# Performance work log

Measured on AMD Instinct MI355X. Metric: run time of the kernel, lower is better.

## Reference

```python
import jax, jax.numpy as jnp
import numpy as np

KERNEL_NUM = 21
SIGMA = 0.1
EXACT_SIGMA = 0.001
EPS = 1e-8  # torch F.cosine_similarity eps


def _kernel_params():
    n = KERNEL_NUM - 1
    mus = [1.0 / n + 2.0 * i / n - 1.0 for i in range(n)] + [1.0]
    sigmas = [SIGMA] * n + [EXACT_SIGMA]
    return jnp.asarray(mus, jnp.float32), jnp.asarray(sigmas, jnp.float32)


def setup_inputs() -> dict:
    key = jax.random.key(0)
    ks = jax.random.split(key, 12)
    B, QL, DL, V, D = 512, 32, 256, 100000, 256
    return {
        "query_1": jax.random.randint(ks[0], (B, QL), 0, V),
        "document_1": jax.random.randint(ks[1], (B, DL), 0, V),
        "query_2": jax.random.randint(ks[2], (B, QL), 0, V),
        "document_2": jax.random.randint(ks[3], (B, DL), 0, V),
        "emb_weight": jax.random.normal(ks[4], (V, D), jnp.float32),
        "W0": jax.random.normal(ks[5], (10, 21), jnp.float32) * 0.2,
        "b0": jax.random.normal(ks[6], (10,), jnp.float32) * 0.1,
        "W1": jax.random.normal(ks[7], (5, 10), jnp.float32) * 0.3,
        "b1": jax.random.normal(ks[8], (5,), jnp.float32) * 0.1,
        "W2": jax.random.normal(ks[9], (1, 5), jnp.float32) * 0.4,
        "b2": jax.random.normal(ks[10], (1,), jnp.float32) * 0.1,
    }


def _predict(query, doc, emb_weight, W0, b0, W1, b1, W2, b2):
    q = emb_weight[query]  # [B, QL, D]
    d = emb_weight[doc]    # [B, DL, D]
    qn = q / jnp.maximum(jnp.linalg.norm(q, axis=-1, keepdims=True), EPS)
    dn = d / jnp.maximum(jnp.linalg.norm(d, axis=-1, keepdims=True), EPS)
    mm = jnp.einsum('bqe,bde->bqd', qn, dn)  # cosine matching matrix [B,QL,DL]
    mus, sigmas = _kernel_params()
    # Gaussian soft binning: [B,QL,DL,K]
    K = jnp.exp(-0.5 * (mm[..., None] - mus) ** 2 / sigmas ** 2)
    km = jnp.log1p(K.sum(axis=2)).sum(axis=1)  # [B, K]
    h = jax.nn.relu(km @ W0.T + b0)
    h = jax.nn.relu(h @ W1.T + b1)
    return h @ W2.T + b2  # [B, 1]


def reference(query_1, document_1, query_2, document_2,
              emb_weight, W0, b0, W1, b1, W2, b2):
    l1 = _predict(query_1, document_1, emb_weight, W0, b0, W1, b1, W2, b2)
    l2 = _predict(query_2, document_2, emb_weight, W0, b0, W1, b1, W2, b2)
    return jax.nn.sigmoid(l1 - l2)
```

## Files before the change

kernel.cpp:

```cpp
#include <hip/hip_runtime.h>
#include <hip/hip_fp8.h>
#include <math.h>

typedef __bf16 bf16x8 __attribute__((ext_vector_type(8)));
typedef __bf16 bf16x4 __attribute__((ext_vector_type(4)));
typedef float  f32x4  __attribute__((ext_vector_type(4)));
typedef float  f32x16 __attribute__((ext_vector_type(16)));

#define QL    32
#define DL    256
#define DIM   256
#define NK    21
#define KSOFT 20
#define STR   264
#define STR8  264
#define L2E   1.4426950408889634f

#if __has_builtin(__builtin_amdgcn_exp2f)
#define EXP2F(x) __builtin_amdgcn_exp2f(x)
#else
#define EXP2F(x) exp2f(x)
#endif

static __device__ inline unsigned cvt2_e4m3(float a, float b)
{
#if __has_builtin(__builtin_amdgcn_cvt_pk_fp8_f32)
    return (unsigned)__builtin_amdgcn_cvt_pk_fp8_f32(a, b, 0, false) & 0xFFFFu;
#else
    __hip_fp8_e4m3 fa(a), fb(b);
    return (unsigned)fa.__x | ((unsigned)fb.__x << 8);
#endif
}

#define EVAL_BINS(mm, ACC0)                                                  \
    {                                                                        \
        float U  = EXP2F(L2E * fmaf(10.0f, (mm), 9.0f));                     \
        float t0 = (mm) + 0.95f;                                             \
        float E  = EXP2F((-50.0f * L2E) * t0 * t0);                          \
        ACC0[0] += E;                                                        \
        E *= U;                           ACC0[1]  += E;          \
        E *= U * 0.36787944117144233f;    ACC0[2]  += E;          \
        E *= U * 0.1353352832366127f;     ACC0[3]  += E;          \
        E *= U * 0.049787068367863944f;   ACC0[4]  += E;          \
        E *= U * 0.018315638888734179f;   ACC0[5]  += E;          \
        E *= U * 0.006737946999085467f;   ACC0[6]  += E;          \
        float t7 = (mm) + 0.25f;                                             \
        E = EXP2F((-50.0f * L2E) * t7 * t7);                                 \
        ACC0[7] += E;                                                        \
        E *= U * 0.0009118819655545162f;  ACC0[8]  += E;          \
        E *= U * 0.00033546262790251185f; ACC0[9]  += E;          \
        E *= U * 0.0001234098040866796f;  ACC0[10] += E;          \
        E *= U * 4.5399929762484854e-05f; ACC0[11] += E;          \
        E *= U * 1.670170079024566e-05f;  ACC0[12] += E;          \
        E *= U * 6.14421235332821e-06f;   ACC0[13] += E;          \
        float t14 = (mm) - 0.45f;                                            \
        E = EXP2F((-50.0f * L2E) * t14 * t14);                               \
        ACC0[14] += E;                                                       \
        E *= U * 8.315287191035679e-07f;  ACC0[15] += E;          \
        E *= U * 3.059023205018258e-07f;  ACC0[16] += E;          \
        E *= U * 1.1253517471925912e-07f; ACC0[17] += E;          \
        E *= U * 4.139937718785167e-08f;  ACC0[18] += E;          \
        E *= U * 1.522997974471263e-08f;  ACC0[19] += E;          \
    }

__global__ __launch_bounds__(256)
void knrm_prep8(const float* __restrict__ emb, unsigned char* __restrict__ tab, int V)
{
    const int wave = threadIdx.x >> 6;
    const int lane = threadIdx.x & 63;
    const int row0 = (blockIdx.x * 4 + wave) * 2;
    if (row0 >= V) return;

    float4 a = reinterpret_cast<const float4*>(emb + (size_t)row0 * DIM)[lane];
    float4 c = reinterpret_cast<const float4*>(emb + (size_t)(row0 + 1) * DIM)[lane];
    float sa = a.x*a.x + a.y*a.y + a.z*a.z + a.w*a.w;
    float sc = c.x*c.x + c.y*c.y + c.z*c.z + c.w*c.w;
    #pragma unroll
    for (int m = 32; m; m >>= 1) { sa += __shfl_xor(sa, m); sc += __shfl_xor(sc, m); }
    float ia = rsqrtf(fmaxf(sa, 1e-16f)) * 16.0f;
    float ic = rsqrtf(fmaxf(sc, 1e-16f)) * 16.0f;
    unsigned pa = cvt2_e4m3(a.x * ia, a.y * ia) | (cvt2_e4m3(a.z * ia, a.w * ia) << 16);
    unsigned pc = cvt2_e4m3(c.x * ic, c.y * ic) | (cvt2_e4m3(c.z * ic, c.w * ic) << 16);
    *reinterpret_cast<unsigned*>(tab + (size_t)row0 * 256 + lane * 4) = pa;
    *reinterpret_cast<unsigned*>(tab + (size_t)(row0 + 1) * 256 + lane * 4) = pc;
}

__global__ __launch_bounds__(256, 2)
void knrm_mainB(const int* __restrict__ q1t, const int* __restrict__ d1t,
                const int* __restrict__ q2t, const int* __restrict__ d2t,
                const unsigned char* __restrict__ tab,
                const float* __restrict__ W0, const float* __restrict__ b0,
                const float* __restrict__ W1, const float* __restrict__ b1,
                const float* __restrict__ W2, const float* __restrict__ b2,
                float* __restrict__ lg, int B)
{
    const int b    = blockIdx.x;
    const int pair = blockIdx.y;
    const int tid  = threadIdx.x;
    const int wave = tid >> 6;
    const int lane = tid & 63;
    const int l31  = lane & 31;
    const int hw   = lane >> 5;

    const int* qtok = pair ? q2t : q1t;
    const int* dtok = pair ? d2t : d1t;

    __shared__ __align__(16) unsigned char qbuf[QL * STR8];
    __shared__ float Sqk[QL * NK];
    __shared__ int   dtok_s[DL];
    __shared__ int   qtok_s[QL];
    __shared__ float km[NK];
    __shared__ float h0[10];
    __shared__ float h1[5];

    if (tid < QL) qtok_s[tid] = qtok[b * QL + tid];
    dtok_s[tid] = dtok[b * DL + tid];
    for (int e = tid; e < QL * NK; e += 256) Sqk[e] = 0.0f;
    if (tid < NK) km[tid] = 0.0f;

    __syncthreads();
    {
        long qv[4];
        #pragma unroll
        for (int i = 0; i < 4; ++i) {
            int r = wave * 8 + i * 2 + hw;
            qv[i] = *reinterpret_cast<const long*>(
                tab + (size_t)qtok_s[r] * 256 + l31 * 8);
        }
        #pragma unroll
        for (int i = 0; i < 4; ++i) {
            int r = wave * 8 + i * 2 + hw;
            *reinterpret_cast<long*>(&qbuf[r * STR8 + l31 * 8]) = qv[i];
        }
    }
    __syncthreads();

    const int qtk1 = qtok_s[l31];

    float acc[NK];
    #pragma unroll
    for (int k = 0; k < NK; ++k) acc[k] = 0.0f;

    const unsigned char* qrd = &qbuf[l31 * STR8 + hw * 8];

    #pragma unroll 1
    for (int t = 0; t < 2; ++t) {
        const int dbase = wave * 64 + t * 32;
        const int tokA  = dtok_s[dbase + l31];
        const unsigned char* abase = tab + (size_t)tokA * 256 + hw * 8;

        long af[16];
        #pragma unroll
        for (int ks = 0; ks < 16; ++ks)
            af[ks] = *reinterpret_cast<const long*>(abase + ks * 16);

        f32x16 mc;
        #pragma unroll
        for (int j = 0; j < 16; ++j) mc[j] = 0.0f;

        #pragma unroll
        for (int ks = 0; ks < 16; ++ks) {
            long bf = *reinterpret_cast<const long*>(qrd + ks * 16);
            mc = __builtin_amdgcn_mfma_f32_32x32x16_fp8_fp8(af[ks], bf, mc, 0, 0, 0);
        }

        #pragma unroll
        for (int r = 0; r < 16; ++r) {
            float mm = mc[r] * 0.00390625f;
            EVAL_BINS(mm, acc);
            int crow = dbase + (r & 3) + 8 * (r >> 2) + 4 * hw;
            acc[KSOFT] += (dtok_s[crow] == qtk1) ? 1.0f : 0.0f;
        }
    }

    #pragma unroll
    for (int k = 0; k < NK; ++k)
        atomicAdd(&Sqk[l31 * NK + k], acc[k]);
    __syncthreads();

    for (int e = tid; e < QL * NK; e += 256)
        atomicAdd(&km[e % NK], log1pf(Sqk[e]));
    __syncthreads();

    if (tid < 10) {
        float h = b0[tid];
        #pragma unroll
        for (int k = 0; k < NK; ++k) h = fmaf(km[k], W0[tid*NK + k], h);
        h0[tid] = fmaxf(h, 0.0f);
    }
    __syncthreads();
    if (tid < 5) {
        float h = b1[tid];
        #pragma unroll
        for (int j = 0; j < 10; ++j) h = fmaf(h0[j], W1[tid*10 + j], h);
        h1[tid] = fmaxf(h, 0.0f);
    }
    __syncthreads();
    if (tid == 0) {
        float l = b2[0];
        #pragma unroll
        for (int j = 0; j < 5; ++j) l = fmaf(h1[j], W2[j], l);
        lg[pair * B + b] = l;
    }
}

__global__ void knrm_final(const float* __restrict__ lg, float* __restrict__ out, int B)
{
    int i = blockIdx.x * 256 + threadIdx.x;
    if (i < B) {
        float z = lg[i] - lg[B + i];
        out[i] = 1.0f / (1.0f + expf(-z));
    }
}

__global__ __launch_bounds__(256, 2)
void knrm_mono(const int* __restrict__ q1t, const int* __restrict__ d1t,
               const int* __restrict__ q2t, const int* __restrict__ d2t,
               const float* __restrict__ emb,
               const float* __restrict__ W0, const float* __restrict__ b0,
               const float* __restrict__ W1, const float* __restrict__ b1,
               const float* __restrict__ W2, const float* __restrict__ b2,
               float* __restrict__ out)
{
    const int b    = blockIdx.x;
    const int tid  = threadIdx.x;
    const int wave = tid >> 6;
    const int lane = tid & 63;
    const int qt   = wave >> 1;
    const int dt   = wave & 1;
    const int g    = lane >> 4;
    const int cl   = lane & 15;

    __shared__ __align__(16) __bf16 qbuf[QL * STR];
    __shared__ __align__(16) __bf16 dbuf[32 * STR];
    __shared__ float Sqk[QL * NK];
    __shared__ int   dtok_s[DL];
    __shared__ int   qtok_s[QL];
    __shared__ float km[NK];
    __shared__ float h0[10];
    __shared__ float h1[5];
    __shared__ float logit[2];

    for (int pair = 0; pair < 2; ++pair) {
        const int* qtok = pair ? q2t : q1t;
        const int* dtok = pair ? d2t : d1t;

        if (tid < QL) qtok_s[tid] = qtok[b * QL + tid];
        dtok_s[tid] = dtok[b * DL + tid];
        for (int e = tid; e < QL * NK; e += 256) Sqk[e] = 0.0f;
        if (tid < NK) km[tid] = 0.0f;
        __syncthreads();

        #pragma unroll
        for (int i = 0; i < 8; ++i) {
            int row = wave * 8 + i;
            int tok = qtok_s[row];
            float4 v = reinterpret_cast<const float4*>(emb + (size_t)tok * DIM)[lane];
            float s = v.x*v.x + v.y*v.y + v.z*v.z + v.w*v.w;
            #pragma unroll
            for (int m = 32; m; m >>= 1) s += __shfl_xor(s, m);
            float inv = rsqrtf(fmaxf(s, 1e-16f));
            bf16x4 o;
            o[0] = (__bf16)(v.x * inv); o[1] = (__bf16)(v.y * inv);
            o[2] = (__bf16)(v.z * inv); o[3] = (__bf16)(v.w * inv);
            *reinterpret_cast<bf16x4*>(&qbuf[row * STR + lane * 4]) = o;
        }

        int qtk[4];
        #pragma unroll
        for (int i = 0; i < 4; ++i) qtk[i] = qtok_s[qt * 16 + g * 4 + i];

        float acc[4 * NK];
        #pragma unroll
        for (int e = 0; e < 4 * NK; ++e) acc[e] = 0.0f;

        for (int tile = 0; tile < 8; ++tile) {
            #pragma unroll
            for (int i = 0; i < 8; ++i) {
                int r = wave * 8 + i;
                int tok = dtok_s[tile * 32 + r];
                float4 v = reinterpret_cast<const float4*>(emb + (size_t)tok * DIM)[lane];
                float s = v.x*v.x + v.y*v.y + v.z*v.z + v.w*v.w;
                #pragma unroll
                for (int m = 32; m; m >>= 1) s += __shfl_xor(s, m);
                float inv = rsqrtf(fmaxf(s, 1e-16f));
                bf16x4 o;
                o[0] = (__bf16)(v.x * inv); o[1] = (__bf16)(v.y * inv);
                o[2] = (__bf16)(v.z * inv); o[3] = (__bf16)(v.w * inv);
                *reinterpret_cast<bf16x4*>(&dbuf[r * STR + lane * 4]) = o;
            }
            __syncthreads();

            f32x4 cf = {0.0f, 0.0f, 0.0f, 0.0f};
            #pragma unroll
            for (int ks = 0; ks < 8; ++ks) {
                bf16x8 af  = *reinterpret_cast<const bf16x8*>(&qbuf[(qt*16 + cl)*STR + ks*32 + g*8]);
                bf16x8 bfr = *reinterpret_cast<const bf16x8*>(&dbuf[(dt*16 + cl)*STR + ks*32 + g*8]);
                cf = __builtin_amdgcn_mfma_f32_16x16x32_bf16(af, bfr, cf, 0, 0, 0);
            }

            int dtk = dtok_s[tile*32 + dt*16 + cl];
            #pragma unroll
            for (int i = 0; i < 4; ++i) {
                float mm = cf[i];
                float* a4 = &acc[i*NK];
                EVAL_BINS(mm, a4);
                a4[KSOFT] += (dtk == qtk[i]) ? 1.0f : 0.0f;
            }
            __syncthreads();
        }

        #pragma unroll
        for (int i = 0; i < 4; ++i) {
            int row = qt*16 + g*4 + i;
            #pragma unroll
            for (int k = 0; k < NK; ++k)
                atomicAdd(&Sqk[row*NK + k], acc[i*NK + k]);
        }
        __syncthreads();

        for (int e = tid; e < QL * NK; e += 256)
            atomicAdd(&km[e % NK], log1pf(Sqk[e]));
        __syncthreads();

        if (tid < 10) {
            float h = b0[tid];
            #pragma unroll
            for (int k = 0; k < NK; ++k) h = fmaf(km[k], W0[tid*NK + k], h);
            h0[tid] = fmaxf(h, 0.0f);
        }
        __syncthreads();
        if (tid < 5) {
            float h = b1[tid];
            #pragma unroll
            for (int j = 0; j < 10; ++j) h = fmaf(h0[j], W1[tid*10 + j], h);
            h1[tid] = fmaxf(h, 0.0f);
        }
        __syncthreads();
        if (tid == 0) {
            float l = b2[0];
            #pragma unroll
            for (int j = 0; j < 5; ++j) l = fmaf(h1[j], W2[j], l);
            logit[pair] = l;
        }
        __syncthreads();
    }

    if (tid == 0) {
        float z = logit[0] - logit[1];
        out[b] = 1.0f / (1.0f + expf(-z));
    }
}

extern "C" void kernel_launch(void* const* d_in, const int* in_sizes, int n_in,
                              void* d_out, int out_size, void* d_ws, size_t ws_size,
                              hipStream_t stream) {
    const int*   q1  = (const int*)d_in[0];
    const int*   d1  = (const int*)d_in[1];
    const int*   q2  = (const int*)d_in[2];
    const int*   d2  = (const int*)d_in[3];
    const float* emb = (const float*)d_in[4];
    const float* W0  = (const float*)d_in[5];
    const float* b0  = (const float*)d_in[6];
    const float* W1  = (const float*)d_in[7];
    const float* b1  = (const float*)d_in[8];
    const float* W2  = (const float*)d_in[9];
    const float* b2  = (const float*)d_in[10];
    float* out = (float*)d_out;

    const int B = in_sizes[0] / QL;
    const int V = in_sizes[4] / DIM;

    size_t tab_bytes = (size_t)V * 256;
    size_t need = tab_bytes + 256 + (size_t)2 * B * sizeof(float);

    if (ws_size >= need) {
        unsigned char* tab = (unsigned char*)d_ws;
        float* lg = (float*)((char*)d_ws + ((tab_bytes + 255) & ~(size_t)255));

        knrm_prep8<<<(V/2 + 3) / 4, 256, 0, stream>>>(emb, tab, V);
        dim3 grid(B, 2);
        knrm_mainB<<<grid, 256, 0, stream>>>(q1, d1, q2, d2, tab,
                                             W0, b0, W1, b1, W2, b2, lg, B);
        knrm_final<<<(B + 255) / 256, 256, 0, stream>>>(lg, out, B);
    } else {
        knrm_mono<<<B, 256, 0, stream>>>(q1, d1, q2, d2, emb,
                                         W0, b0, W1, b1, W2, b2, out);
    }
}
```

Baseline: 229.8 us.

## Split document dimension across blocks with global atomic accumulation and separate reduce kernel

The main kernel now splits each query/doc pair's 256 document tokens across two blocks via a third grid dimension. Each wave handles one 32-row tile, and the document fragment loads are hoisted ahead of the query staging. Per-block Sqk partials are atomically added into a global buffer that the prep kernel zeroes. A new reduce kernel applies log1p, runs the MLP for both pairs and writes the sigmoid, which removes the old final kernel. This doubles block count for better occupancy and latency hiding, at the cost of global atomics, extra workspace traffic and redundant query staging per block.

After: 246.4 us. 1.07x slower.

```diff
diff --git a/kernel.cpp b/kernel.cpp
--- a/kernel.cpp
+++ b/kernel.cpp
@@ -64,8 +64,13 @@
     }
 
 __global__ __launch_bounds__(256)
-void knrm_prep8(const float* __restrict__ emb, unsigned char* __restrict__ tab, int V)
+void knrm_prep8(const float* __restrict__ emb, unsigned char* __restrict__ tab,
+                int V, float* __restrict__ sqkg, int sqkn)
 {
+    {
+        int idx = blockIdx.x * 256 + threadIdx.x;
+        if (idx < sqkn) sqkg[idx] = 0.0f;
+    }
     const int wave = threadIdx.x >> 6;
     const int lane = threadIdx.x & 63;
     const int row0 = (blockIdx.x * 4 + wave) * 2;
@@ -86,16 +91,14 @@
 }
 
 __global__ __launch_bounds__(256, 2)
-void knrm_mainB(const int* __restrict__ q1t, const int* __restrict__ d1t,
+void knrm_mainC(const int* __restrict__ q1t, const int* __restrict__ d1t,
                 const int* __restrict__ q2t, const int* __restrict__ d2t,
                 const unsigned char* __restrict__ tab,
-                const float* __restrict__ W0, const float* __restrict__ b0,
-                const float* __restrict__ W1, const float* __restrict__ b1,
-                const float* __restrict__ W2, const float* __restrict__ b2,
-                float* __restrict__ lg, int B)
+                float* __restrict__ sqkg, int B)
 {
     const int b    = blockIdx.x;
     const int pair = blockIdx.y;
+    const int z    = blockIdx.z;
     const int tid  = threadIdx.x;
     const int wave = tid >> 6;
     const int lane = tid & 63;
@@ -107,18 +110,22 @@
 
     __shared__ __align__(16) unsigned char qbuf[QL * STR8];
     __shared__ float Sqk[QL * NK];
-    __shared__ int   dtok_s[DL];
+    __shared__ int   dtok_s[128];
     __shared__ int   qtok_s[QL];
-    __shared__ float km[NK];
-    __shared__ float h0[10];
-    __shared__ float h1[5];
-
-    if (tid < QL) qtok_s[tid] = qtok[b * QL + tid];
-    dtok_s[tid] = dtok[b * DL + tid];
+
+    if (tid < QL)  qtok_s[tid] = qtok[b * QL + tid];
+    if (tid < 128) dtok_s[tid] = dtok[b * DL + z * 128 + tid];
     for (int e = tid; e < QL * NK; e += 256) Sqk[e] = 0.0f;
-    if (tid < NK) km[tid] = 0.0f;
-
-    __syncthreads();
+    __syncthreads();
+
+    const int dloc = wave * 32;
+    const int tokA = dtok_s[dloc + l31];
+    const unsigned char* abase = tab + (size_t)tokA * 256 + hw * 8;
+    long af[16];
+    #pragma unroll
+    for (int ks = 0; ks < 16; ++ks)
+        af[ks] = *reinterpret_cast<const long*>(abase + ks * 16);
+
     {
         long qv[4];
         #pragma unroll
@@ -136,41 +143,27 @@
     __syncthreads();
 
     const int qtk1 = qtok_s[l31];
+    const unsigned char* qrd = &qbuf[l31 * STR8 + hw * 8];
 
     float acc[NK];
     #pragma unroll
     for (int k = 0; k < NK; ++k) acc[k] = 0.0f;
 
-    const unsigned char* qrd = &qbuf[l31 * STR8 + hw * 8];
-
-    #pragma unroll 1
-    for (int t = 0; t < 2; ++t) {
-        const int dbase = wave * 64 + t * 32;
-        const int tokA  = dtok_s[dbase + l31];
-        const unsigned char* abase = tab + (size_t)tokA * 256 + hw * 8;
-
-        long af[16];
-        #pragma unroll
-        for (int ks = 0; ks < 16; ++ks)
-            af[ks] = *reinterpret_cast<const long*>(abase + ks * 16);
-
-        f32x16 mc;
-        #pragma unroll
-        for (int j = 0; j < 16; ++j) mc[j] = 0.0f;
-
-        #pragma unroll
-        for (int ks = 0; ks < 16; ++ks) {
-            long bf = *reinterpret_cast<const long*>(qrd + ks * 16);
-            mc = __builtin_amdgcn_mfma_f32_32x32x16_fp8_fp8(af[ks], bf, mc, 0, 0, 0);
-        }
-
-        #pragma unroll
-        for (int r = 0; r < 16; ++r) {
-            float mm = mc[r] * 0.00390625f;
-            EVAL_BINS(mm, acc);
-            int crow = dbase + (r & 3) + 8 * (r >> 2) + 4 * hw;
-            acc[KSOFT] += (dtok_s[crow] == qtk1) ? 1.0f : 0.0f;
-        }
+    f32x16 mc;
+    #pragma unroll
+    for (int j = 0; j < 16; ++j) mc[j] = 0.0f;
+    #pragma unroll
+    for (int ks = 0; ks < 16; ++ks) {
+        long bf = *reinterpret_cast<const long*>(qrd + ks * 16);
+        mc = __builtin_amdgcn_mfma_f32_32x32x16_fp8_fp8(af[ks], bf, mc, 0, 0, 0);
+    }
+
+    #pragma unroll
+    for (int r = 0; r < 16; ++r) {
+        float mm = mc[r] * 0.00390625f;
+        EVAL_BINS(mm, acc);
+        int crow = dloc + (r & 3) + 8 * (r >> 2) + 4 * hw;
+        acc[KSOFT] += (dtok_s[crow] == qtk1) ? 1.0f : 0.0f;
     }
 
     #pragma unroll
@@ -178,38 +171,61 @@
         atomicAdd(&Sqk[l31 * NK + k], acc[k]);
     __syncthreads();
 
+    float* dst = sqkg + (size_t)(b * 2 + pair) * (QL * NK);
     for (int e = tid; e < QL * NK; e += 256)
-        atomicAdd(&km[e % NK], log1pf(Sqk[e]));
-    __syncthreads();
-
-    if (tid < 10) {
-        float h = b0[tid];
-        #pragma unroll
-        for (int k = 0; k < NK; ++k) h = fmaf(km[k], W0[tid*NK + k], h);
-        h0[tid] = fmaxf(h, 0.0f);
-    }
-    __syncthreads();
-    if (tid < 5) {
-        float h = b1[tid];
-        #pragma unroll
-        for (int j = 0; j < 10; ++j) h = fmaf(h0[j], W1[tid*10 + j], h);
-        h1[tid] = fmaxf(h, 0.0f);
-    }
-    __syncthreads();
-    if (tid == 0) {
+        atomicAdd(&dst[e], Sqk[e]);
+}
+
+__global__ __launch_bounds__(64)
+void knrm_red(const float* __restrict__ sqkg,
+              const float* __restrict__ W0, const float* __restrict__ b0,
+              const float* __restrict__ W1, const float* __restrict__ b1,
+              const float* __restrict__ W2, const float* __restrict__ b2,
+              float* __restrict__ out, int B)
+{
+    const int b = blockIdx.x;
+    const int t = threadIdx.x;
+
+    __shared__ float km[2][NK];
+    __shared__ float h0[2][10];
+    __shared__ float h1[2][5];
+    __shared__ float lgs[2];
+
+    if (t < 2 * NK) {
+        int pair = t / NK, k = t % NK;
+        const float* src = sqkg + (size_t)(b * 2 + pair) * (QL * NK);
+        float s = 0.0f;
+        #pragma unroll
+        for (int q = 0; q < QL; ++q) s += log1pf(src[q * NK + k]);
+        km[pair][k] = s;
+    }
+    __syncthreads();
+    if (t < 20) {
+        int pair = t / 10, i = t % 10;
+        float h = b0[i];
+        #pragma unroll
+        for (int k = 0; k < NK; ++k) h = fmaf(km[pair][k], W0[i*NK + k], h);
+        h0[pair][i] = fmaxf(h, 0.0f);
+    }
+    __syncthreads();
+    if (t < 10) {
+        int pair = t / 5, i = t % 5;
+        float h = b1[i];
+        #pragma unroll
+        for (int j = 0; j < 10; ++j) h = fmaf(h0[pair][j], W1[i*10 + j], h);
+        h1[pair][i] = fmaxf(h, 0.0f);
+    }
+    __syncthreads();
+    if (t < 2) {
         float l = b2[0];
         #pragma unroll
-        for (int j = 0; j < 5; ++j) l = fmaf(h1[j], W2[j], l);
-        lg[pair * B + b] = l;
-    }
-}
-
-__global__ void knrm_final(const float* __restrict__ lg, float* __restrict__ out, int B)
-{
-    int i = blockIdx.x * 256 + threadIdx.x;
-    if (i < B) {
-        float z = lg[i] - lg[B + i];
-        out[i] = 1.0f / (1.0f + expf(-z));
+        for (int j = 0; j < 5; ++j) l = fmaf(h1[t][j], W2[j], l);
+        lgs[t] = l;
+    }
+    __syncthreads();
+    if (t == 0) {
+        float z = lgs[0] - lgs[1];
+        out[b] = 1.0f / (1.0f + expf(-z));
     }
 }
 
@@ -372,17 +388,17 @@
     const int V = in_sizes[4] / DIM;
 
     size_t tab_bytes = (size_t)V * 256;
-    size_t need = tab_bytes + 256 + (size_t)2 * B * sizeof(float);
+    int    sqkn      = B * 2 * QL * NK;
+    size_t need = tab_bytes + 256 + (size_t)sqkn * sizeof(float);
 
     if (ws_size >= need) {
         unsigned char* tab = (unsigned char*)d_ws;
-        float* lg = (float*)((char*)d_ws + ((tab_bytes + 255) & ~(size_t)255));
-
-        knrm_prep8<<<(V/2 + 3) / 4, 256, 0, stream>>>(emb, tab, V);
-        dim3 grid(B, 2);
-        knrm_mainB<<<grid, 256, 0, stream>>>(q1, d1, q2, d2, tab,
-                                             W0, b0, W1, b1, W2, b2, lg, B);
-        knrm_final<<<(B + 255) / 256, 256, 0, stream>>>(lg, out, B);
+        float* sqkg = (float*)((char*)d_ws + ((tab_bytes + 255) & ~(size_t)255));
+
+        knrm_prep8<<<(V/2 + 3) / 4, 256, 0, stream>>>(emb, tab, V, sqkg, sqkn);
+        dim3 grid(B, 2, 2);
+        knrm_mainC<<<grid, 256, 0, stream>>>(q1, d1, q2, d2, tab, sqkg, B);
+        knrm_red<<<B, 64, 0, stream>>>(sqkg, W0, b0, W1, b1, W2, b2, out, B);
     } else {
         knrm_mono<<<B, 256, 0, stream>>>(q1, d1, q2, d2, emb,
                                          W0, b0, W1, b1, W2, b2, out);
```
